# Kernel optimization log

Measured on AMD Instinct MI355X. Metric: run time of the kernel, lower is better.

## Reference

```python
import jax, jax.numpy as jnp
import numpy as np
from jax import lax


def setup_inputs() -> dict:
    key = jax.random.key(0)
    ks = jax.random.split(key, 6)
    T, B, I, H = 512, 64, 1024, 1024
    f16 = jnp.float16
    # scale weights down so fp16 activations stay in range
    return {
        "x": jax.random.normal(ks[0], (T, B, I), dtype=f16),
        "h0": jax.random.normal(ks[1], (1, B, H), dtype=f16),
        "w_ih": (jax.random.normal(ks[2], (3 * H, I), dtype=f16) * f16(0.02)),
        "w_hh": (jax.random.normal(ks[3], (3 * H, H), dtype=f16) * f16(0.02)),
        "b_ih": jax.random.normal(ks[4], (3 * H,), dtype=f16),
        "b_hh": jax.random.normal(ks[5], (3 * H,), dtype=f16),
    }


def reference(x, h0, w_ih, w_hh, b_ih, b_hh):
    # Single-layer GRU forward, PyTorch gate order (r, z, n).
    # fp16 storage, fp32 accumulation, hidden state re-quantized to fp16
    # each timestep (matches the fused CUDA kernel's shared-memory half buffer).
    f32 = jnp.float32
    H = h0.shape[-1]
    wih = w_ih.astype(f32)   # (3H, I)
    whh = w_hh.astype(f32)   # (3H, H)
    bih = b_ih.astype(f32)
    bhh = b_hh.astype(f32)

    # Precompute input-projection for all timesteps: (T, B, 3H)
    gi = jnp.einsum('tbi,gi->tbg', x.astype(f32), wih) + bih

    def step(h_prev16, gi_t):
        h_prev = h_prev16.astype(f32)                       # (B, H)
        gh = h_prev @ whh.T + bhh                           # (B, 3H)
        ir, iz, inn = gi_t[:, :H], gi_t[:, H:2 * H], gi_t[:, 2 * H:]
        hr, hz, hn = gh[:, :H], gh[:, H:2 * H], gh[:, 2 * H:]
        r = jax.nn.sigmoid(ir + hr)
        z = jax.nn.sigmoid(iz + hz)
        n = jnp.tanh(inn + r * hn)
        h_new = ((1.0 - z) * n + z * h_prev).astype(jnp.float16)
        return h_new, h_new

    _, y = lax.scan(step, h0[0], gi)                        # y: (T, B, H) fp16
    return y
```

## Files before the change

kernel.cpp:

```cpp
#include <hip/hip_runtime.h>
#include <hip/hip_bf16.h>
#include <hip/hip_fp16.h>


typedef __attribute__((ext_vector_type(8))) _Float16 f16x8;
typedef __attribute__((ext_vector_type(4))) float f32x4;
typedef __attribute__((ext_vector_type(8))) float f32x8;

#define MFMA(a, b, c) __builtin_amdgcn_mfma_f32_16x16x32_f16((a), (b), (c), 0, 0, 0)

#define T_T 512
#define T_B 64
#define T_K 1024
#define T_N3 3072

__device__ float          g_gi[(size_t)T_T * T_B * T_N3];
__device__ unsigned short g_hbf[(size_t)T_T * T_B * T_K];
__device__ unsigned       g_flags[64 * 32];

static __device__ __forceinline__ f16x8 cvt8(f32x8 v) {
    f16x8 r;
    #pragma unroll
    for (int i = 0; i < 8; ++i) r[i] = (_Float16)v[i];
    return r;
}
static __device__ __forceinline__ float sigmoidf_(float x) {
    return 1.0f / (1.0f + __expf(-x));
}
static __device__ __forceinline__ float tanhf_(float x) {
    return 2.0f / (1.0f + __expf(-2.0f * x)) - 1.0f;
}

__global__ __launch_bounds__(256) void reset_flags_k() {
    for (int i = threadIdx.x; i < 64 * 32; i += 256) g_flags[i] = 0;
}

__global__ __launch_bounds__(256) void gi_gemm(
    const float* __restrict__ X,
    const float* __restrict__ W,
    const float* __restrict__ bih)
{
    __shared__ unsigned short lA[128 * 32];
    __shared__ unsigned short lB[128 * 32];
    const int tid  = threadIdx.x;
    const int lane = tid & 63;
    const int wid  = tid >> 6;
    const int m0 = (blockIdx.x / 24) * 128;
    const int n0 = (blockIdx.x % 24) * 128;
    const int wm = wid >> 1, wn = wid & 1;

    f32x4 acc[4][4] = {};

    for (int k0 = 0; k0 < T_K; k0 += 32) {
        #pragma unroll
        for (int i = 0; i < 2; ++i) {
            int idx = tid + i * 256;
            int kc  = idx & 3;
            int row = idx >> 2;
            f32x8 va = *(const f32x8*)(X + (size_t)(m0 + row) * T_K + k0 + kc * 8);
            f32x8 vb = *(const f32x8*)(W + (size_t)(n0 + row) * T_K + k0 + kc * 8);
            *(f16x8*)((char*)lA + kc * 2048 + row * 16) = cvt8(va);
            *(f16x8*)((char*)lB + kc * 2048 + row * 16) = cvt8(vb);
        }
        __syncthreads();

        f16x8 a[4], b[4];
        #pragma unroll
        for (int mt = 0; mt < 4; ++mt) {
            int row = 64 * wm + 16 * mt + (lane & 15);
            a[mt] = *(const f16x8*)((const char*)lA + (lane >> 4) * 2048 + row * 16);
        }
        #pragma unroll
        for (int nt = 0; nt < 4; ++nt) {
            int row = 64 * wn + 16 * nt + (lane & 15);
            b[nt] = *(const f16x8*)((const char*)lB + (lane >> 4) * 2048 + row * 16);
        }
        #pragma unroll
        for (int mt = 0; mt < 4; ++mt)
            #pragma unroll
            for (int nt = 0; nt < 4; ++nt)
                acc[mt][nt] = MFMA(a[mt], b[nt], acc[mt][nt]);
        __syncthreads();
    }

    #pragma unroll
    for (int mt = 0; mt < 4; ++mt) {
        int rbase = m0 + 64 * wm + 16 * mt + (lane >> 4) * 4;
        #pragma unroll
        for (int nt = 0; nt < 4; ++nt) {
            int col = n0 + 64 * wn + 16 * nt + (lane & 15);
            float bv = bih[col];
            #pragma unroll
            for (int j = 0; j < 4; ++j)
                g_gi[(size_t)(rbase + j) * T_N3 + col] = acc[mt][nt][j] + bv;
        }
    }
}

__global__ __launch_bounds__(256, 1) void gru_scan(
    const float* __restrict__ Whh,
    const float* __restrict__ Bhh,
    const float* __restrict__ H0,
    float* Y)
{
    __shared__ unsigned short Wl[48 * 1024];
    const int tid  = threadIdx.x;
    const int lane = tid & 63;
    const int w    = tid >> 6;
    const int c0   = blockIdx.x * 16;

    for (int idx = tid; idx < 48 * 128; idx += 256) {
        int row = idx >> 7;
        int kc  = idx & 127;
        int gate = row >> 4, cc = row & 15;
        f32x8 v = *(const f32x8*)(Whh + (size_t)(gate * 1024 + c0 + cc) * T_K + kc * 8);
        *(f16x8*)((char*)Wl + kc * 768 + row * 16) = cvt8(v);
    }
    const int colL = c0 + (lane & 15);
    const float br = Bhh[colL];
    const float bz = Bhh[1024 + colL];
    const float bn = Bhh[2048 + colL];
    __syncthreads();

    const char* bbase = (const char*)Wl + (lane >> 4) * 768 + (lane & 15) * 16;

    float pr[4], pz[4], pn[4];
    #pragma unroll
    for (int j = 0; j < 4; ++j) {
        int row = 16 * w + (lane >> 4) * 4 + j;
        pr[j] = g_gi[(size_t)row * T_N3 + colL];
        pz[j] = g_gi[(size_t)row * T_N3 + 1024 + colL];
        pn[j] = g_gi[(size_t)row * T_N3 + 2048 + colL];
    }

    float hreg[4];

    for (int t = 0; t < T_T; ++t) {
        f32x4 ar = {0.f, 0.f, 0.f, 0.f}, az = ar, an = ar;

        if (t == 0) {
            const float* abase =
                H0 + (size_t)(16 * w + (lane & 15)) * T_K + (lane >> 4) * 8;
            #pragma unroll 4
            for (int kk = 0; kk < 32; ++kk) {
                f16x8 af = cvt8(*(const f32x8*)(abase + kk * 32));
                const char* bb = bbase + kk * 3072;
                ar = MFMA(af, *(const f16x8*)(bb),       ar);
                az = MFMA(af, *(const f16x8*)(bb + 256), az);
                an = MFMA(af, *(const f16x8*)(bb + 512), an);
            }
        } else {
            const unsigned short* abase = g_hbf + (size_t)(t - 1) * (T_B * T_K)
                + (size_t)(16 * w + (lane & 15)) * T_K + (lane >> 4) * 8;
            f16x8 af[32];
            #pragma unroll
            for (int kk = 0; kk < 32; ++kk)
                af[kk] = *(const f16x8*)(abase + kk * 32);
            #pragma unroll
            for (int kk = 0; kk < 32; ++kk) {
                const char* bb = bbase + kk * 3072;
                ar = MFMA(af[kk], *(const f16x8*)(bb),       ar);
                az = MFMA(af[kk], *(const f16x8*)(bb + 256), az);
                an = MFMA(af[kk], *(const f16x8*)(bb + 512), an);
            }
        }

        #pragma unroll
        for (int j = 0; j < 4; ++j) {
            int row = 16 * w + (lane >> 4) * 4 + j;
            size_t off = (size_t)row * T_K + colL;
            float hp = (t == 0) ? H0[off] : hreg[j];
            float r = sigmoidf_(pr[j] + ar[j] + br);
            float z = sigmoidf_(pz[j] + az[j] + bz);
            float n = tanhf_(pn[j] + r * (an[j] + bn));
            float h = (1.0f - z) * n + z * hp;
            __half h16 = __float2half(h);
            float  hq  = __half2float(h16);
            hreg[j] = hq;
            Y[(size_t)t * (T_B * T_K) + off] = hq;

            unsigned v16 = (unsigned)__half_as_ushort(h16);
            unsigned up  = __shfl_xor(v16, 1);
            if (!(lane & 1)) {
                unsigned packed = v16 | (up << 16);
                unsigned* dst = (unsigned*)(g_hbf + (size_t)t * (T_B * T_K) + off);
                __hip_atomic_store(dst, packed, __ATOMIC_RELAXED,
                                   __HIP_MEMORY_SCOPE_AGENT);
            }
        }

        if (t + 1 < T_T) {
            asm volatile("s_waitcnt vmcnt(0)" ::: "memory");
            __syncthreads();
            if (tid == 0)
                __hip_atomic_store(&g_flags[blockIdx.x * 32], (unsigned)(t + 1),
                                   __ATOMIC_RELAXED, __HIP_MEMORY_SCOPE_AGENT);

            const float* g = g_gi + (size_t)(t + 1) * T_B * T_N3;
            #pragma unroll
            for (int j = 0; j < 4; ++j) {
                int row = 16 * w + (lane >> 4) * 4 + j;
                pr[j] = g[(size_t)row * T_N3 + colL];
                pz[j] = g[(size_t)row * T_N3 + 1024 + colL];
                pn[j] = g[(size_t)row * T_N3 + 2048 + colL];
            }

            if (w == 0) {
                unsigned tgt = (unsigned)(t + 1);
                for (;;) {
                    unsigned v = __hip_atomic_load(&g_flags[lane * 32],
                                                   __ATOMIC_RELAXED,
                                                   __HIP_MEMORY_SCOPE_AGENT);
                    if (__all((int)(v >= tgt))) break;
                    __builtin_amdgcn_s_sleep(1);
                }
            }
            asm volatile("" ::: "memory");
            __syncthreads();
        }
    }
}

extern "C" void kernel_launch(void* const* d_in, const int* in_sizes, int n_in,
                              void* d_out, int out_size, void* d_ws, size_t ws_size,
                              hipStream_t stream)
{
    const float* X   = (const float*)d_in[0];
    const float* H0  = (const float*)d_in[1];
    const float* Wih = (const float*)d_in[2];
    const float* Whh = (const float*)d_in[3];
    const float* Bih = (const float*)d_in[4];
    const float* Bhh = (const float*)d_in[5];
    float* Y = (float*)d_out;
    (void)d_ws; (void)ws_size; (void)in_sizes; (void)n_in; (void)out_size;

    reset_flags_k<<<dim3(1), dim3(256), 0, stream>>>();

    gi_gemm<<<dim3(256 * 24), dim3(256), 0, stream>>>(X, Wih, Bih);

    gru_scan<<<dim3(64), dim3(256), 0, stream>>>(Whh, Bhh, H0, Y);
}
```

Before: 4.968 ms.

## Replace per-block flag barrier with per-wave per-timestep arrival counters

```diff
diff --git a/kernel.cpp b/kernel.cpp
--- a/kernel.cpp
+++ b/kernel.cpp
@@ -16,7 +16,7 @@
 
 __device__ float          g_gi[(size_t)T_T * T_B * T_N3];
 __device__ unsigned short g_hbf[(size_t)T_T * T_B * T_K];
-__device__ unsigned       g_flags[64 * 32];
+__device__ unsigned       g_ctr[(size_t)T_T * 4 * 32];
 
 static __device__ __forceinline__ f16x8 cvt8(f32x8 v) {
     f16x8 r;
@@ -32,7 +32,7 @@
 }
 
 __global__ __launch_bounds__(256) void reset_flags_k() {
-    for (int i = threadIdx.x; i < 64 * 32; i += 256) g_flags[i] = 0;
+    for (int i = threadIdx.x; i < T_T * 4 * 32; i += 256) g_ctr[i] = 0;
 }
 
 __global__ __launch_bounds__(256) void gi_gemm(
@@ -152,16 +152,13 @@
         } else {
             const unsigned short* abase = g_hbf + (size_t)(t - 1) * (T_B * T_K)
                 + (size_t)(16 * w + (lane & 15)) * T_K + (lane >> 4) * 8;
-            f16x8 af[32];
-            #pragma unroll
-            for (int kk = 0; kk < 32; ++kk)
-                af[kk] = *(const f16x8*)(abase + kk * 32);
-            #pragma unroll
+            #pragma unroll 8
             for (int kk = 0; kk < 32; ++kk) {
+                f16x8 af = *(const f16x8*)(abase + kk * 32);
                 const char* bb = bbase + kk * 3072;
-                ar = MFMA(af[kk], *(const f16x8*)(bb),       ar);
-                az = MFMA(af[kk], *(const f16x8*)(bb + 256), az);
-                an = MFMA(af[kk], *(const f16x8*)(bb + 512), an);
+                ar = MFMA(af, *(const f16x8*)(bb),       ar);
+                az = MFMA(af, *(const f16x8*)(bb + 256), az);
+                an = MFMA(af, *(const f16x8*)(bb + 512), an);
             }
         }
 
@@ -177,7 +174,6 @@
             __half h16 = __float2half(h);
             float  hq  = __half2float(h16);
             hreg[j] = hq;
-            Y[(size_t)t * (T_B * T_K) + off] = hq;
 
             unsigned v16 = (unsigned)__half_as_ushort(h16);
             unsigned up  = __shfl_xor(v16, 1);
@@ -189,13 +185,23 @@
             }
         }
 
+        unsigned* ctr = &g_ctr[((size_t)t * 4 + w) * 32];
+
         if (t + 1 < T_T) {
             asm volatile("s_waitcnt vmcnt(0)" ::: "memory");
-            __syncthreads();
-            if (tid == 0)
-                __hip_atomic_store(&g_flags[blockIdx.x * 32], (unsigned)(t + 1),
-                                   __ATOMIC_RELAXED, __HIP_MEMORY_SCOPE_AGENT);
-
+            if (lane == 0)
+                __hip_atomic_fetch_add(ctr, 1u, __ATOMIC_RELAXED,
+                                       __HIP_MEMORY_SCOPE_AGENT);
+        }
+
+        #pragma unroll
+        for (int j = 0; j < 4; ++j) {
+            int row = 16 * w + (lane >> 4) * 4 + j;
+            size_t off = (size_t)row * T_K + colL;
+            Y[(size_t)t * (T_B * T_K) + off] = hreg[j];
+        }
+
+        if (t + 1 < T_T) {
             const float* g = g_gi + (size_t)(t + 1) * T_B * T_N3;
             #pragma unroll
             for (int j = 0; j < 4; ++j) {
@@ -205,18 +211,16 @@
                 pn[j] = g[(size_t)row * T_N3 + 2048 + colL];
             }
 
-            if (w == 0) {
-                unsigned tgt = (unsigned)(t + 1);
-                for (;;) {
-                    unsigned v = __hip_atomic_load(&g_flags[lane * 32],
-                                                   __ATOMIC_RELAXED,
-                                                   __HIP_MEMORY_SCOPE_AGENT);
-                    if (__all((int)(v >= tgt))) break;
-                    __builtin_amdgcn_s_sleep(1);
-                }
+            for (;;) {
+                unsigned v = 0;
+                if (lane == 0)
+                    v = __hip_atomic_load(ctr, __ATOMIC_RELAXED,
+                                          __HIP_MEMORY_SCOPE_AGENT);
+                v = __shfl(v, 0);
+                if (v >= 64u) break;
+                __builtin_amdgcn_s_sleep(1);
             }
             asm volatile("" ::: "memory");
-            __syncthreads();
         }
     }
 }
```

Measured after the change: 7.740 ms. 1.56x slower.
